# Performance work log

Measured on AMD Instinct MI355X. Metric: run time of the kernel, lower is better.

## Reference

```python
import jax, jax.numpy as jnp
import numpy as np

DPSI_THRESHOLD = 0.05
MSE_WEIGHT = 10.0
LOGIT_EPS = 1e-7
N = 8192


def setup_inputs() -> dict:
    key = jax.random.key(0)
    k1, k2 = jax.random.split(key)
    pred_psi_val = jax.random.normal(k1, (N,), dtype=jnp.float32)
    psi_val = jax.random.uniform(k2, (N,), dtype=jnp.float32)
    return {"pred_psi_val": pred_psi_val, "psi_val": psi_val, "use_BCE_loss_only": 0}


def _bce_with_logits(logits, targets):
    # numerically stable BCE-with-logits, mean reduction
    return jnp.mean(jnp.maximum(logits, 0.0) - logits * targets
                    + jnp.log1p(jnp.exp(-jnp.abs(logits))))


def _logit(p, eps):
    # torch.special.logit(p, eps): clamp p to [eps, 1-eps] then log(p/(1-p))
    p = jnp.clip(p, eps, 1.0 - eps)
    return jnp.log(p) - jnp.log1p(-p)


def reference(pred_psi_val, psi_val, use_BCE_loss_only):
    loss = _bce_with_logits(pred_psi_val, psi_val)
    if use_BCE_loss_only:  # static python flag
        return loss
    psi_logit = _logit(psi_val, LOGIT_EPS)
    # all-pairs differences [N, N]
    pred_diff = pred_psi_val[:, None] - pred_psi_val[None, :]
    true_diff = psi_logit[:, None] - psi_logit[None, :]
    ori_true_diff = psi_val[:, None] - psi_val[None, :]
    valid = jnp.abs(ori_true_diff) >= DPSI_THRESHOLD
    n_valid = jnp.sum(valid)
    sq = jnp.where(valid, (pred_diff - true_diff) ** 2, 0.0)
    pairwise_mse = jnp.sum(sq) / jnp.maximum(n_valid, 1).astype(sq.dtype)
    # add pairwise term only if at least one valid pair exists
    return jnp.where(n_valid > 0, loss + MSE_WEIGHT * pairwise_mse, loss)
```

## Files before the change

### kernel.cpp

```cpp
#include <hip/hip_runtime.h>


constexpr float DPSI_T   = 0.05f;
constexpr float LOGIT_EPS = 1e-7f;

__device__ __forceinline__ float logit_f(float p) {
    p = fminf(fmaxf(p, LOGIT_EPS), 1.0f - LOGIT_EPS);
    return logf(p) - log1pf(-p);
}

__global__ __launch_bounds__(256) void pair_kernel(const float* __restrict__ pred,
                                                   const float* __restrict__ psi,
                                                   float* __restrict__ part_sum,
                                                   unsigned int* __restrict__ part_cnt,
                                                   int n) {
    __shared__ float2 tile[256];
    const int tid = threadIdx.x;
    const float NANF = __int_as_float(0x7fc00000);

    int j = blockIdx.y * 256 + tid;
    if (j < n) {
        float pj = psi[j];
        tile[tid] = make_float2(pj, pred[j] - logit_f(pj));
    } else {
        tile[tid] = make_float2(NANF, 0.0f);
    }

    int i = blockIdx.x * 256 + tid;
    float psi_i, d_i;
    if (i < n) {
        psi_i = psi[i];
        d_i   = pred[i] - logit_f(psi_i);
    } else {
        psi_i = NANF;
        d_i   = 0.0f;
    }
    __syncthreads();

    float sum = 0.0f;
    unsigned int cnt = 0;
    #pragma unroll 8
    for (int k = 0; k < 256; ++k) {
        float2 t   = tile[k];
        float dpsi = psi_i - t.x;
        bool valid = fabsf(dpsi) >= DPSI_T;
        float dd   = d_i - t.y;
        float ddm  = valid ? dd : 0.0f;
        sum = fmaf(ddm, ddm, sum);
        cnt += valid ? 1u : 0u;
    }

    for (int off = 32; off; off >>= 1) {
        sum += __shfl_down(sum, off);
        cnt += __shfl_down(cnt, off);
    }
    __shared__ float wsum[4];
    __shared__ unsigned int wcnt[4];
    int wave = tid >> 6, lane = tid & 63;
    if (lane == 0) { wsum[wave] = sum; wcnt[wave] = cnt; }
    __syncthreads();
    if (tid == 0) {
        float s = wsum[0] + wsum[1] + wsum[2] + wsum[3];
        unsigned int c = wcnt[0] + wcnt[1] + wcnt[2] + wcnt[3];
        int slot = blockIdx.x * gridDim.y + blockIdx.y;
        part_sum[slot] = s;
        part_cnt[slot] = c;
    }
}

__global__ __launch_bounds__(256) void finalize_kernel(const float* __restrict__ pred,
                                                       const float* __restrict__ psi,
                                                       const int* __restrict__ flag,
                                                       const float* __restrict__ part_sum,
                                                       const unsigned int* __restrict__ part_cnt,
                                                       int nparts,
                                                       float* __restrict__ out,
                                                       int n) {
    const int tid = threadIdx.x;

    float bce = 0.0f;
    for (int i = tid; i < n; i += 256) {
        float x = pred[i], t = psi[i];
        bce += fmaxf(x, 0.0f) - x * t + log1pf(expf(-fabsf(x)));
    }
    float s = 0.0f;
    unsigned long long c = 0;
    for (int p = tid; p < nparts; p += 256) {
        s += part_sum[p];
        c += (unsigned long long)part_cnt[p];
    }

    for (int off = 32; off; off >>= 1) {
        bce += __shfl_down(bce, off);
        s   += __shfl_down(s, off);
        c   += __shfl_down(c, off);
    }
    __shared__ float b4[4], s4[4];
    __shared__ unsigned long long c4[4];
    int wave = tid >> 6, lane = tid & 63;
    if (lane == 0) { b4[wave] = bce; s4[wave] = s; c4[wave] = c; }
    __syncthreads();
    if (tid == 0) {
        float bce_total = (b4[0] + b4[1] + b4[2] + b4[3]) / (float)n;
        float s_total   = s4[0] + s4[1] + s4[2] + s4[3];
        unsigned long long c_total = c4[0] + c4[1] + c4[2] + c4[3];
        float loss = bce_total;
        if (flag[0] == 0 && c_total > 0) {
            loss += 10.0f * (s_total / (float)c_total);
        }
        out[0] = loss;
    }
}

extern "C" void kernel_launch(void* const* d_in, const int* in_sizes, int n_in,
                              void* d_out, int out_size, void* d_ws, size_t ws_size,
                              hipStream_t stream) {
    const float* pred = (const float*)d_in[0];
    const float* psi  = (const float*)d_in[1];
    const int*   flag = (const int*)d_in[2];
    float* out = (float*)d_out;
    int n = in_sizes[0];

    int nb = (n + 255) / 256;
    int nparts = nb * nb;
    float* part_sum        = (float*)d_ws;
    unsigned int* part_cnt = (unsigned int*)((char*)d_ws + (size_t)nparts * sizeof(float));

    dim3 grid(nb, nb);
    pair_kernel<<<grid, 256, 0, stream>>>(pred, psi, part_sum, part_cnt, n);
    finalize_kernel<<<1, 256, 0, stream>>>(pred, psi, flag, part_sum, part_cnt, nparts, out, n);
}
```

Measured before the change: 82.48 us.

## Register-block four rows per thread and count valid pairs with wave ballots

Each thread now handles four rows against a smaller 128-column shared tile, so every LDS read of a column value is reused across four rows. The per-lane valid counter and its shuffle reduction are replaced by a wave-wide ballot plus popcount per comparison. The grid shape changes so there are fewer row blocks and more column blocks. The aim is to cut LDS traffic and integer counting per pair. The cost is a scalar popcount in the inner loop and more register pressure.

Result: no change. 82.65 us (+0.2%).

```diff
diff --git a/kernel.cpp b/kernel.cpp
--- a/kernel.cpp
+++ b/kernel.cpp
@@ -1,8 +1,11 @@
 #include <hip/hip_runtime.h>
 
 
-constexpr float DPSI_T   = 0.05f;
+constexpr float DPSI_T    = 0.05f;
 constexpr float LOGIT_EPS = 1e-7f;
+constexpr int   CB  = 128;
+constexpr int   RPT = 4;
+constexpr int   TPB = 256;
 
 __device__ __forceinline__ float logit_f(float p) {
     p = fminf(fmaxf(p, LOGIT_EPS), 1.0f - LOGIT_EPS);
@@ -14,57 +17,66 @@
                                                    float* __restrict__ part_sum,
                                                    unsigned int* __restrict__ part_cnt,
                                                    int n) {
-    __shared__ float2 tile[256];
+    __shared__ float2 tile[CB];
     const int tid = threadIdx.x;
     const float NANF = __int_as_float(0x7fc00000);
 
-    int j = blockIdx.y * 256 + tid;
-    if (j < n) {
-        float pj = psi[j];
-        tile[tid] = make_float2(pj, pred[j] - logit_f(pj));
-    } else {
-        tile[tid] = make_float2(NANF, 0.0f);
+    if (tid < CB) {
+        int j = blockIdx.y * CB + tid;
+        if (j < n) {
+            float pj = psi[j];
+            tile[tid] = make_float2(pj, pred[j] - logit_f(pj));
+        } else {
+            tile[tid] = make_float2(NANF, 0.0f);
+        }
     }
 
-    int i = blockIdx.x * 256 + tid;
-    float psi_i, d_i;
-    if (i < n) {
-        psi_i = psi[i];
-        d_i   = pred[i] - logit_f(psi_i);
-    } else {
-        psi_i = NANF;
-        d_i   = 0.0f;
+    float psi_i[RPT], d_i[RPT];
+    const int rbase = blockIdx.x * (TPB * RPT);
+    #pragma unroll
+    for (int r = 0; r < RPT; ++r) {
+        int i = rbase + r * TPB + tid;
+        if (i < n) {
+            float pi = psi[i];
+            psi_i[r] = pi;
+            d_i[r]   = pred[i] - logit_f(pi);
+        } else {
+            psi_i[r] = NANF;
+            d_i[r]   = 0.0f;
+        }
     }
     __syncthreads();
 
-    float sum = 0.0f;
-    unsigned int cnt = 0;
+    float sum[RPT] = {0.0f, 0.0f, 0.0f, 0.0f};
+    unsigned int cntw = 0;
     #pragma unroll 8
-    for (int k = 0; k < 256; ++k) {
-        float2 t   = tile[k];
-        float dpsi = psi_i - t.x;
-        bool valid = fabsf(dpsi) >= DPSI_T;
-        float dd   = d_i - t.y;
-        float ddm  = valid ? dd : 0.0f;
-        sum = fmaf(ddm, ddm, sum);
-        cnt += valid ? 1u : 0u;
+    for (int k = 0; k < CB; ++k) {
+        float2 t = tile[k];
+        #pragma unroll
+        for (int r = 0; r < RPT; ++r) {
+            float dpsi = psi_i[r] - t.x;
+            bool  v    = fabsf(dpsi) >= DPSI_T;
+            float dd   = d_i[r] - t.y;
+            float ddm  = v ? dd : 0.0f;
+            sum[r] = fmaf(ddm, ddm, sum[r]);
+            cntw += (unsigned int)__popcll(__ballot(v));
+        }
     }
 
-    for (int off = 32; off; off >>= 1) {
-        sum += __shfl_down(sum, off);
-        cnt += __shfl_down(cnt, off);
-    }
+    float s = (sum[0] + sum[1]) + (sum[2] + sum[3]);
+    for (int off = 32; off; off >>= 1) s += __shfl_down(s, off);
+
     __shared__ float wsum[4];
     __shared__ unsigned int wcnt[4];
     int wave = tid >> 6, lane = tid & 63;
-    if (lane == 0) { wsum[wave] = sum; wcnt[wave] = cnt; }
+    if (lane == 0) { wsum[wave] = s; wcnt[wave] = cntw; }
     __syncthreads();
     if (tid == 0) {
-        float s = wsum[0] + wsum[1] + wsum[2] + wsum[3];
-        unsigned int c = wcnt[0] + wcnt[1] + wcnt[2] + wcnt[3];
+        float st = (wsum[0] + wsum[1]) + (wsum[2] + wsum[3]);
+        unsigned int ct = wcnt[0] + wcnt[1] + wcnt[2] + wcnt[3];
         int slot = blockIdx.x * gridDim.y + blockIdx.y;
-        part_sum[slot] = s;
-        part_cnt[slot] = c;
+        part_sum[slot] = st;
+        part_cnt[slot] = ct;
     }
 }
 
@@ -102,7 +114,7 @@
     __syncthreads();
     if (tid == 0) {
         float bce_total = (b4[0] + b4[1] + b4[2] + b4[3]) / (float)n;
-        float s_total   = s4[0] + s4[1] + s4[2] + s4[3];
+        float s_total   = (s4[0] + s4[1]) + (s4[2] + s4[3]);
         unsigned long long c_total = c4[0] + c4[1] + c4[2] + c4[3];
         float loss = bce_total;
         if (flag[0] == 0 && c_total > 0) {
@@ -121,12 +133,13 @@
     float* out = (float*)d_out;
     int n = in_sizes[0];
 
-    int nb = (n + 255) / 256;
-    int nparts = nb * nb;
+    int nbr = (n + TPB * RPT - 1) / (TPB * RPT);
+    int nbc = (n + CB - 1) / CB;
+    int nparts = nbr * nbc;
     float* part_sum        = (float*)d_ws;
     unsigned int* part_cnt = (unsigned int*)((char*)d_ws + (size_t)nparts * sizeof(float));
 
-    dim3 grid(nb, nb);
-    pair_kernel<<<grid, 256, 0, stream>>>(pred, psi, part_sum, part_cnt, n);
+    dim3 grid(nbr, nbc);
+    pair_kernel<<<grid, TPB, 0, stream>>>(pred, psi, part_sum, part_cnt, n);
     finalize_kernel<<<1, 256, 0, stream>>>(pred, psi, flag, part_sum, part_cnt, nparts, out, n);
 }
```
